# Kernel tuning notes

Hardware: AMD Instinct MI355X
Metric: run time of the kernel (lower is better)

The kernel has to match this reference:

```python
import jax, jax.numpy as jnp
from jax import lax
import numpy as np

H, W_DIM = 4096, 4096
KH, KW = 2, 2


def setup_inputs() -> dict:
    key = jax.random.key(0)
    kx, kw = jax.random.split(key)
    X = jax.random.normal(kx, (H, W_DIM), dtype=jnp.float32)
    W = jax.random.uniform(kw, (KH, KW), dtype=jnp.float32)
    return {"X": X, "W": W}


def _conv_valid(X, W):
    # VALID 2D cross-correlation: Y[i,j] = sum_{a,b} X[i+a, j+b] * W[a,b]
    x = X[None, None]          # [1,1,H,W]
    k = W[None, None]          # [1,1,kh,kw]
    y = lax.conv_general_dilated(x, k, window_strides=(1, 1), padding='VALID')
    return y[0, 0]             # [H-kh+1, W-kw+1]


def _trans_conv(X, W):
    # Transposed conv (scatter-add of X[i,j]*W) == full *convolution* with W,
    # i.e. cross-correlation with the spatially flipped kernel, padding kh-1/kw-1.
    x = X[None, None]
    k = W[::-1, ::-1][None, None]
    y = lax.conv_general_dilated(x, k, window_strides=(1, 1),
                                 padding=[(KH - 1, KH - 1), (KW - 1, KW - 1)])
    return y[0, 0]             # back to [H, W]


def reference(X, W):
    y1 = _conv_valid(X, W)     # [H-1, W-1]
    y2 = _trans_conv(y1, W)    # [H, W]
    return y2
```

## Files before the change

### kernel.cpp

```cpp
#include <hip/hip_runtime.h>


#define HD 4096
#define QPR (HD / 4)

__global__ __launch_bounds__(256) void fused_conv_kernel(
    const float* __restrict__ X, const float* __restrict__ Wk,
    float* __restrict__ Y)
{
    const int idx = blockIdx.x * blockDim.x + threadIdx.x;
    const int i  = idx >> 10;
    const int j0 = (idx & (QPR - 1)) << 2;
    if (i >= HD) return;

    const float w00 = Wk[0], w01 = Wk[1], w10 = Wk[2], w11 = Wk[3];

    float x[3][6];
    #pragma unroll
    for (int r = 0; r < 3; ++r) {
        const int row = i - 1 + r;
        if (row >= 0 && row < HD) {
            const float* rp = X + (size_t)row * HD;
            const float4 v = *reinterpret_cast<const float4*>(rp + j0);
            x[r][1] = v.x; x[r][2] = v.y; x[r][3] = v.z; x[r][4] = v.w;
            x[r][0] = (j0 > 0)      ? rp[j0 - 1] : 0.f;
            x[r][5] = (j0 + 4 < HD) ? rp[j0 + 4] : 0.f;
        } else {
            #pragma unroll
            for (int c = 0; c < 6; ++c) x[r][c] = 0.f;
        }
    }

    float y1v[2][5];
    #pragma unroll
    for (int p = 0; p < 2; ++p) {
        const int prow = i - 1 + p;
        const bool pv = (prow >= 0) && (prow < HD - 1);
        #pragma unroll
        for (int q = 0; q < 5; ++q) {
            const int qcol = j0 - 1 + q;
            const bool qv = (qcol >= 0) && (qcol < HD - 1);
            const float v = w00 * x[p][q]     + w01 * x[p][q + 1]
                          + w10 * x[p + 1][q] + w11 * x[p + 1][q + 1];
            y1v[p][q] = (pv && qv) ? v : 0.f;
        }
    }

    float4 out;
    out.x = w00 * y1v[1][1] + w01 * y1v[1][0] + w10 * y1v[0][1] + w11 * y1v[0][0];
    out.y = w00 * y1v[1][2] + w01 * y1v[1][1] + w10 * y1v[0][2] + w11 * y1v[0][1];
    out.z = w00 * y1v[1][3] + w01 * y1v[1][2] + w10 * y1v[0][3] + w11 * y1v[0][2];
    out.w = w00 * y1v[1][4] + w01 * y1v[1][3] + w10 * y1v[0][4] + w11 * y1v[0][3];
    *reinterpret_cast<float4*>(Y + (size_t)i * HD + j0) = out;
}

extern "C" void kernel_launch(void* const* d_in, const int* in_sizes, int n_in,
                              void* d_out, int out_size, void* d_ws, size_t ws_size,
                              hipStream_t stream) {
    const float* X  = (const float*)d_in[0];
    const float* Wk = (const float*)d_in[1];
    float* Y        = (float*)d_out;

    const int total_threads = HD * QPR;
    const int block = 256;
    const int grid  = total_threads / block;
    fused_conv_kernel<<<grid, block, 0, stream>>>(X, Wk, Y);
}
```

Baseline: 126.6 us.

## Process 8 output rows per thread with rolling row and intermediate reuse

Each thread now produces a column strip of 8 consecutive output rows instead of one. It keeps the previous input row and the previous intermediate conv row in registers and slides them down, so each input row is loaded about once per thread instead of three times, and the first-stage conv is computed once per row instead of twice. The grid shrinks by 8x, which lowers the number of threads available to hide memory latency.

```diff
diff --git a/kernel.cpp b/kernel.cpp
--- a/kernel.cpp
+++ b/kernel.cpp
@@ -2,56 +2,81 @@
 
 
 #define HD 4096
-#define QPR (HD / 4)
+#define QPR 1024
+#define RB 8
+
+__device__ __forceinline__ void load_row(const float* __restrict__ X, int row,
+                                         int j0, float x[6]) {
+    if (row >= 0 && row < HD) {
+        const float* rp = X + (size_t)row * HD;
+        const float4 v = *reinterpret_cast<const float4*>(rp + j0);
+        x[1] = v.x; x[2] = v.y; x[3] = v.z; x[4] = v.w;
+        x[0] = (j0 > 0)      ? rp[j0 - 1] : 0.f;
+        x[5] = (j0 + 4 < HD) ? rp[j0 + 4] : 0.f;
+    } else {
+        #pragma unroll
+        for (int c = 0; c < 6; ++c) x[c] = 0.f;
+    }
+}
 
 __global__ __launch_bounds__(256) void fused_conv_kernel(
     const float* __restrict__ X, const float* __restrict__ Wk,
     float* __restrict__ Y)
 {
-    const int idx = blockIdx.x * blockDim.x + threadIdx.x;
-    const int i  = idx >> 10;
-    const int j0 = (idx & (QPR - 1)) << 2;
-    if (i >= HD) return;
+    const int idx  = blockIdx.x * blockDim.x + threadIdx.x;
+    const int i0   = (idx >> 10) * RB;
+    const int j0   = (idx & (QPR - 1)) << 2;
 
     const float w00 = Wk[0], w01 = Wk[1], w10 = Wk[2], w11 = Wk[3];
 
-    float x[3][6];
+    bool qv[5];
     #pragma unroll
-    for (int r = 0; r < 3; ++r) {
-        const int row = i - 1 + r;
-        if (row >= 0 && row < HD) {
-            const float* rp = X + (size_t)row * HD;
-            const float4 v = *reinterpret_cast<const float4*>(rp + j0);
-            x[r][1] = v.x; x[r][2] = v.y; x[r][3] = v.z; x[r][4] = v.w;
-            x[r][0] = (j0 > 0)      ? rp[j0 - 1] : 0.f;
-            x[r][5] = (j0 + 4 < HD) ? rp[j0 + 4] : 0.f;
-        } else {
-            #pragma unroll
-            for (int c = 0; c < 6; ++c) x[r][c] = 0.f;
+    for (int q = 0; q < 5; ++q) {
+        const int qc = j0 - 1 + q;
+        qv[q] = (qc >= 0) && (qc < HD - 1);
+    }
+
+    float xa[6], xb[6];
+    load_row(X, i0 - 1, j0, xa);
+    load_row(X, i0,     j0, xb);
+
+    float y1p[5];
+    {
+        const bool pv = (i0 - 1 >= 0);
+        #pragma unroll
+        for (int q = 0; q < 5; ++q) {
+            const float v = w00 * xa[q] + w01 * xa[q + 1]
+                          + w10 * xb[q] + w11 * xb[q + 1];
+            y1p[q] = (pv && qv[q]) ? v : 0.f;
         }
     }
 
-    float y1v[2][5];
     #pragma unroll
-    for (int p = 0; p < 2; ++p) {
-        const int prow = i - 1 + p;
-        const bool pv = (prow >= 0) && (prow < HD - 1);
+    for (int r = 0; r < RB; ++r) {
+        const int i = i0 + r;
+        load_row(X, i + 1, j0, xa);
+
+        float y1c[5];
+        const bool pv = (i < HD - 1);
         #pragma unroll
         for (int q = 0; q < 5; ++q) {
-            const int qcol = j0 - 1 + q;
-            const bool qv = (qcol >= 0) && (qcol < HD - 1);
-            const float v = w00 * x[p][q]     + w01 * x[p][q + 1]
-                          + w10 * x[p + 1][q] + w11 * x[p + 1][q + 1];
-            y1v[p][q] = (pv && qv) ? v : 0.f;
+            const float v = w00 * xb[q] + w01 * xb[q + 1]
+                          + w10 * xa[q] + w11 * xa[q + 1];
+            y1c[q] = (pv && qv[q]) ? v : 0.f;
         }
+
+        float4 out;
+        out.x = w00 * y1c[1] + w01 * y1c[0] + w10 * y1p[1] + w11 * y1p[0];
+        out.y = w00 * y1c[2] + w01 * y1c[1] + w10 * y1p[2] + w11 * y1p[1];
+        out.z = w00 * y1c[3] + w01 * y1c[2] + w10 * y1p[3] + w11 * y1p[2];
+        out.w = w00 * y1c[4] + w01 * y1c[3] + w10 * y1p[4] + w11 * y1p[3];
+        *reinterpret_cast<float4*>(Y + (size_t)i * HD + j0) = out;
+
+        #pragma unroll
+        for (int q = 0; q < 5; ++q) y1p[q] = y1c[q];
+        #pragma unroll
+        for (int c = 0; c < 6; ++c) xb[c] = xa[c];
     }
-
-    float4 out;
-    out.x = w00 * y1v[1][1] + w01 * y1v[1][0] + w10 * y1v[0][1] + w11 * y1v[0][0];
-    out.y = w00 * y1v[1][2] + w01 * y1v[1][1] + w10 * y1v[0][2] + w11 * y1v[0][1];
-    out.z = w00 * y1v[1][3] + w01 * y1v[1][2] + w10 * y1v[0][3] + w11 * y1v[0][2];
-    out.w = w00 * y1v[1][4] + w01 * y1v[1][3] + w10 * y1v[0][4] + w11 * y1v[0][3];
-    *reinterpret_cast<float4*>(Y + (size_t)i * HD + j0) = out;
 }
 
 extern "C" void kernel_launch(void* const* d_in, const int* in_sizes, int n_in,
@@ -61,7 +86,7 @@
     const float* Wk = (const float*)d_in[1];
     float* Y        = (float*)d_out;
 
-    const int total_threads = HD * QPR;
+    const int total_threads = (HD / RB) * QPR;
     const int block = 256;
     const int grid  = total_threads / block;
     fused_conv_kernel<<<grid, block, 0, stream>>>(X, Wk, Y);
```

Result: faster. 120.1 us (-5.1%).
